# Kernel tuning notes

Measured on AMD Instinct MI355X. Metric: run time of the kernel, lower is better.

The kernel has to match this reference:

```python
import jax, jax.numpy as jnp
import numpy as np

B, S, HID = 2, 2048, 2048
H, KV, D = 16, 8, 128          # query heads, kv heads, head dim
NREP = H // KV
EPS = 1e-6
THETA = 1000000.0
SCALE = 1.0 / np.sqrt(D)


def setup_inputs() -> dict:
    key = jax.random.key(0)
    ks = jax.random.split(key, 5)
    x = jax.random.normal(ks[0], (B, S, HID), jnp.float32)
    std = 0.02
    Wq = jax.random.normal(ks[1], (HID, H * D), jnp.float32) * std
    Wk = jax.random.normal(ks[2], (HID, KV * D), jnp.float32) * std
    Wv = jax.random.normal(ks[3], (HID, KV * D), jnp.float32) * std
    Wo = jax.random.normal(ks[4], (H * D, HID), jnp.float32) * std
    q_norm_w = jnp.ones((D,), jnp.float32)
    k_norm_w = jnp.ones((D,), jnp.float32)
    # standard RoPE cos/sin table: [S, D]
    inv_freq = 1.0 / (THETA ** (jnp.arange(0, D, 2, dtype=jnp.float32) / D))
    freqs = jnp.arange(S, dtype=jnp.float32)[:, None] * inv_freq[None, :]
    emb = jnp.concatenate([freqs, freqs], axis=-1)
    return {"x": x, "Wq": Wq, "Wk": Wk, "Wv": Wv, "Wo": Wo,
            "q_norm_w": q_norm_w, "k_norm_w": k_norm_w,
            "cos": jnp.cos(emb), "sin": jnp.sin(emb)}


def _rmsnorm(x, w, eps=EPS):
    var = jnp.mean(jnp.square(x), axis=-1, keepdims=True)
    return w * (x * jax.lax.rsqrt(var + eps))


def _rotate_half(x):
    x1, x2 = jnp.split(x, 2, axis=-1)
    return jnp.concatenate([-x2, x1], axis=-1)


def _rope(t, cos, sin):
    # t: [B, h, S, D]; cos/sin: [S, D]
    return t * cos[None, None] + _rotate_half(t) * sin[None, None]


def reference(x, Wq, Wk, Wv, Wo, q_norm_w, k_norm_w, cos, sin):
    q = (x @ Wq).reshape(B, S, H, D)
    k = (x @ Wk).reshape(B, S, KV, D)
    v = (x @ Wv).reshape(B, S, KV, D)
    q = _rmsnorm(q, q_norm_w).transpose(0, 2, 1, 3)   # [B, H, S, D]
    k = _rmsnorm(k, k_norm_w).transpose(0, 2, 1, 3)   # [B, KV, S, D]
    v = v.transpose(0, 2, 1, 3)                       # [B, KV, S, D]
    q = _rope(q, cos, sin)
    k = _rope(k, cos, sin)
    # GQA without materializing repeated K/V: group q heads per kv head
    qg = q.reshape(B, KV, NREP, S, D)
    scores = jnp.einsum('bgrsd,bgtd->bgrst', qg, k) * SCALE  # [B,KV,NREP,S,S]
    causal = jnp.tril(jnp.ones((S, S), dtype=bool))
    scores = jnp.where(causal, scores, jnp.finfo(scores.dtype).min)
    p = jax.nn.softmax(scores, axis=-1)
    out = jnp.einsum('bgrst,bgtd->bgrsd', p, v).reshape(B, H, S, D)
    out = out.transpose(0, 2, 1, 3).reshape(B, S, H * D)
    return out @ Wo
```

## Files before the change

kernel.cpp:

```cpp
#include <hip/hip_runtime.h>

typedef unsigned short u16;
typedef __bf16 bf16x8 __attribute__((ext_vector_type(8)));
typedef float f32x4 __attribute__((ext_vector_type(4)));

#define Bn 2
#define Sn 2048
#define HIDn 2048
#define Hn 16
#define KVn 8
#define Dn 128
#define SCALEf 0.08838834764831845f

__device__ __forceinline__ float b2f(u16 v) {
  return __builtin_bit_cast(float, (unsigned)v << 16);
}
__device__ __forceinline__ u16 f2b(float f) {
  unsigned u = __builtin_bit_cast(unsigned, f);
  u += 0x7fffu + ((u >> 16) & 1u);
  return (u16)(u >> 16);
}
__device__ __forceinline__ bool is_bf16(const void* det) {
  return *(const unsigned*)det == 0x3F803F80u;
}
__device__ __forceinline__ float ldx(const void* p, long i, bool isbf) {
  return isbf ? b2f(((const u16*)p)[i]) : ((const float*)p)[i];
}
__device__ __forceinline__ void gl_lds16(const u16* g, u16* l) {
  __builtin_amdgcn_global_load_lds(
      (unsigned int __attribute__((address_space(1)))*)g,
      (unsigned int __attribute__((address_space(3)))*)l, 16, 0, 0);
}

template <int CTRL>
__device__ __forceinline__ float dpp_mov(float x) {
  return __builtin_bit_cast(
      float, __builtin_amdgcn_update_dpp(0, __builtin_bit_cast(int, x), CTRL,
                                         0xF, 0xF, true));
}
__device__ __forceinline__ float red16_max(float x) {
  x = fmaxf(x, dpp_mov<0xB1>(x));
  x = fmaxf(x, dpp_mov<0x4E>(x));
  x = fmaxf(x, dpp_mov<0x141>(x));
  x = fmaxf(x, dpp_mov<0x140>(x));
  return x;
}
__device__ __forceinline__ float red16_sum(float x) {
  x += dpp_mov<0xB1>(x);
  x += dpp_mov<0x4E>(x);
  x += dpp_mov<0x141>(x);
  x += dpp_mov<0x140>(x);
  return x;
}

__global__ __launch_bounds__(256) void convert_x(
    const void* __restrict__ in, u16* __restrict__ out, const void* __restrict__ det) {
  bool isbf = is_bf16(det);
  long i = ((long)blockIdx.x * 256 + threadIdx.x) * 4;
  if (isbf) {
    *(ushort4*)(out + i) = *(const ushort4*)((const u16*)in + i);
  } else {
    float4 f = *(const float4*)((const float*)in + i);
    out[i] = f2b(f.x); out[i + 1] = f2b(f.y); out[i + 2] = f2b(f.z); out[i + 3] = f2b(f.w);
  }
}

__global__ __launch_bounds__(256) void transpose_any(
    const void* __restrict__ vin, u16* __restrict__ out, const void* __restrict__ det,
    int irs, int ors, long ib0, long ob0, int nb1, long ib1, long ob1) {
  __shared__ u16 tile[64][65];
  bool isbf = det ? is_bf16(det) : true;
  int bz = blockIdx.z;
  long ibase = (long)(bz / nb1) * ib0 + (long)(bz % nb1) * ib1;
  u16* op = out + (long)(bz / nb1) * ob0 + (long)(bz % nb1) * ob1;
  long r0 = (long)blockIdx.y * 64, c0 = (long)blockIdx.x * 64;
  int t = threadIdx.x;
  int tr = t >> 3, tc = (t & 7) * 8;
#pragma unroll
  for (int p = 0; p < 2; ++p) {
    int r = p * 32 + tr;
    long src = ibase + (r0 + r) * irs + c0 + tc;
    if (isbf) {
      const u16* ip = (const u16*)vin;
#pragma unroll
      for (int j = 0; j < 8; ++j) tile[r][tc + j] = ip[src + j];
    } else {
      const float* ip = (const float*)vin;
#pragma unroll
      for (int j = 0; j < 8; ++j) tile[r][tc + j] = f2b(ip[src + j]);
    }
  }
  __syncthreads();
#pragma unroll
  for (int p = 0; p < 2; ++p) {
    int r = p * 32 + tr;
    u16* dst = op + (c0 + r) * ors + r0 + tc;
#pragma unroll
    for (int j = 0; j < 8; ++j) dst[j] = tile[tc + j][r];
  }
}

__global__ __launch_bounds__(256) void gemm_bt(
    const u16* __restrict__ A, const u16* __restrict__ Bt, u16* __restrict__ C,
    float* __restrict__ Cf, const void* __restrict__ det, int N, int K) {
  __shared__ alignas(16) u16 As[128 * 64];
  __shared__ alignas(16) u16 Bs[128 * 64];
  int t = threadIdx.x;
  int wave = t >> 6, lane = t & 63, quad = lane >> 4, l15 = lane & 15;
  long bm = (long)blockIdx.y * 128, bn = (long)blockIdx.x * 128;
  int wm = (wave >> 1) * 64, wn = (wave & 1) * 64;
  f32x4 acc[4][4] = {};
  int sg = ((t & 7) ^ ((t >> 3) & 7)) * 8;
  const u16* Ab = A + (bm + (t >> 3)) * K + sg;
  const u16* Bb = Bt + (bn + (t >> 3)) * K + sg;
  for (int k0 = 0; k0 < K; k0 += 64) {
    __syncthreads();
#pragma unroll
    for (int p = 0; p < 4; ++p) {
      gl_lds16(Ab + (long)(p * 32) * K + k0, As + p * 2048 + t * 8);
      gl_lds16(Bb + (long)(p * 32) * K + k0, Bs + p * 2048 + t * 8);
    }
    __syncthreads();
#pragma unroll
    for (int kt = 0; kt < 2; ++kt) {
      int fg = ((kt * 4 + quad) ^ (l15 & 7)) * 8;
      bf16x8 a[4], b[4];
#pragma unroll
      for (int i = 0; i < 4; ++i)
        a[i] = *(const bf16x8*)(As + (wm + i * 16 + l15) * 64 + fg);
#pragma unroll
      for (int j = 0; j < 4; ++j)
        b[j] = *(const bf16x8*)(Bs + (wn + j * 16 + l15) * 64 + fg);
#pragma unroll
      for (int i = 0; i < 4; ++i)
#pragma unroll
        for (int j = 0; j < 4; ++j)
          acc[i][j] = __builtin_amdgcn_mfma_f32_16x16x32_bf16(a[i], b[j], acc[i][j], 0, 0, 0);
    }
  }
  bool tofloat = (Cf != nullptr) && !is_bf16(det);
#pragma unroll
  for (int i = 0; i < 4; ++i) {
    long row = bm + wm + i * 16 + quad * 4;
#pragma unroll
    for (int j = 0; j < 4; ++j) {
      long col = bn + wn + j * 16 + l15;
      if (tofloat) {
#pragma unroll
        for (int r = 0; r < 4; ++r) Cf[(row + r) * N + col] = acc[i][j][r];
      } else {
#pragma unroll
        for (int r = 0; r < 4; ++r) C[(row + r) * N + col] = f2b(acc[i][j][r]);
      }
    }
  }
}

__global__ __launch_bounds__(512, 2) void gemm_qkv256(
    const u16* __restrict__ A, const u16* __restrict__ Bt,
    u16* __restrict__ Qout, u16* __restrict__ Kout, u16* __restrict__ Vout,
    const void* __restrict__ qw, const void* __restrict__ kw,
    const void* __restrict__ cosb, const void* __restrict__ sinb, int K) {
  __shared__ alignas(16) u16 As[2][2][8192];
  __shared__ alignas(16) u16 Bs[2][2][8192];
  const int NT = K >> 6;
  bool isbf = is_bf16(qw);
  int t = threadIdx.x;
  int wave = t >> 6, lane = t & 63, quad = lane >> 4, l15 = lane & 15;
  int l7 = l15 & 7;
  int wmi = wave >> 1, wni = wave & 1;
  long bm = (long)blockIdx.y * 256;
  long bn = (long)blockIdx.x * 256;
  int s0 = t, s1 = t + 512;
  int r0 = s0 >> 3, r1 = s1 >> 3;
  int gs0 = (s0 & 7) ^ (r0 & 7), gs1 = (s1 & 7) ^ (r1 & 7);
  const u16* Ab0 = A + bm * K;
  const u16* Ab1 = A + (bm + 128) * K;
  const u16* Bb0 = Bt + bn * K;
  const u16* Bb1 = Bt + (bn + 128) * K;
#define STG(dst, src)                                          \
  gl_lds16((src) + (long)r0 * K + gs0 * 8, (dst) + s0 * 8);    \
  gl_lds16((src) + (long)r1 * K + gs1 * 8, (dst) + s1 * 8);
#define FENCE asm volatile("" ::: "memory")
  int ah = wmi >> 1;
  int arb = (wmi & 1) * 64 + l15;
#define LDA(m, kk) (*(const bf16x8*)(Ah + (arb + (m)*16) * 64 + ((((kk)*4 + quad) ^ l7) * 8)))
#define LDB(n, kk) (*(const bf16x8*)(Bh + ((n)*16 + l15) * 64 + ((((kk)*4 + quad) ^ l7) * 8)))
  f32x4 acc[4][8] = {};
  STG((u16*)As[0][0], Ab0);
  STG((u16*)As[0][1], Ab1);
  STG((u16*)Bs[0][0], Bb0);
  STG((u16*)Bs[0][1], Bb1);
  STG((u16*)As[1][0], Ab0 + 64);
  STG((u16*)As[1][1], Ab1 + 64);
  asm volatile("s_waitcnt vmcnt(4)" ::: "memory");
  __builtin_amdgcn_s_barrier();

  for (int tk = 0; tk < NT; ++tk) {
    const u16* Ah = (const u16*)As[tk & 1][ah];
    const u16* Bh = (const u16*)Bs[tk & 1][wni];
    u16* BsN0 = (u16*)Bs[(tk + 1) & 1][0];
    u16* BsN1 = (u16*)Bs[(tk + 1) & 1][1];
    u16* AsN0 = (u16*)As[tk & 1][0];
    u16* AsN1 = (u16*)As[tk & 1][1];
    bf16x8 aa[4], bb[4];
#pragma unroll
    for (int m = 0; m < 4; ++m) aa[m] = LDA(m, 0);
#pragma unroll
    for (int j = 0; j < 4; ++j) bb[j] = LDB(j, 0);
    if (tk + 1 < NT) { STG(BsN0, Bb0 + (tk + 1) * 64); }
    FENCE; __builtin_amdgcn_s_barrier();
    asm volatile("s_waitcnt lgkmcnt(0)" ::: "memory");
    __builtin_amdgcn_s_setprio(1);
#pragma unroll
    for (int m = 0; m < 4; ++m)
#pragma unroll
      for (int j = 0; j < 4; ++j)
        acc[m][j] = __builtin_amdgcn_mfma_f32_16x16x32_bf16(aa[m], bb[j], acc[m][j], 0, 0, 0);
    __builtin_amdgcn_s_setprio(0);
    FENCE; __builtin_amdgcn_s_barrier();
#pragma unroll
    for (int j = 0; j < 4; ++j) bb[j] = LDB(j + 4, 0);
    if (tk + 1 < NT) { STG(BsN1, Bb1 + (tk + 1) * 64); }
    FENCE; __builtin_amdgcn_s_barrier();
    asm volatile("s_waitcnt lgkmcnt(0)" ::: "memory");
    __builtin_amdgcn_s_setprio(1);
#pragma unroll
    for (int m = 0; m < 4; ++m)
#pragma unroll
      for (int j = 0; j < 4; ++j)
        acc[m][j + 4] = __builtin_amdgcn_mfma_f32_16x16x32_bf16(aa[m], bb[j], acc[m][j + 4], 0, 0, 0);
    __builtin_amdgcn_s_setprio(0);
    FENCE; __builtin_amdgcn_s_barrier();
#pragma unroll
    for (int m = 0; m < 4; ++m) aa[m] = LDA(m, 1);
#pragma unroll
    for (int j = 0; j < 4; ++j) bb[j] = LDB(j, 1);
    FENCE; __builtin_amdgcn_s_barrier();
    asm volatile("s_waitcnt lgkmcnt(0)" ::: "memory");
    __builtin_amdgcn_s_setprio(1);
#pragma unroll
    for (int m = 0; m < 4; ++m)
#pragma unroll
      for (int j = 0; j < 4; ++j)
        acc[m][j] = __builtin_amdgcn_mfma_f32_16x16x32_bf16(aa[m], bb[j], acc[m][j], 0, 0, 0);
    __builtin_amdgcn_s_setprio(0);
    FENCE; __builtin_amdgcn_s_barrier();
#pragma unroll
    for (int j = 0; j < 4; ++j) bb[j] = LDB(j + 4, 1);
    if (tk + 2 < NT) {
      STG(AsN0, Ab0 + (tk + 2) * 64);
      STG(AsN1, Ab1 + (tk + 2) * 64);
      asm volatile("s_waitcnt vmcnt(4)" ::: "memory");
    } else {
      asm volatile("s_waitcnt vmcnt(0)" ::: "memory");
    }
    __builtin_amdgcn_s_barrier();
    asm volatile("s_waitcnt lgkmcnt(0)" ::: "memory");
    __builtin_amdgcn_s_setprio(1);
#pragma unroll
    for (int m = 0; m < 4; ++m)
#pragma unroll
      for (int j = 0; j < 4; ++j)
        acc[m][j + 4] = __builtin_amdgcn_mfma_f32_16x16x32_bf16(aa[m], bb[j], acc[m][j + 4], 0, 0, 0);
    __builtin_amdgcn_s_setprio(0);
    FENCE; __builtin_amdgcn_s_barrier();
  }
#undef STG
#undef LDA
#undef LDB
#undef FENCE
  int hglob = (int)(bn >> 7) + wni;
  int mrow0 = (int)bm + wmi * 64 + quad * 4;
  if (hglob < Hn + KVn) {
    bool isq = hglob < Hn;
    const void* w = isq ? qw : kw;
    int nh = isq ? Hn : KVn;
    int hh = isq ? hglob : hglob - Hn;
    u16* Ob = isq ? Qout : Kout;
#pragma unroll
    for (int m = 0; m < 4; ++m) {
#pragma unroll
      for (int r = 0; r < 4; ++r) {
        float ss = 0.f;
#pragma unroll
        for (int j = 0; j < 8; ++j) { float v = acc[m][j][r]; ss += v * v; }
        ss = red16_sum(ss);
        float scale = rsqrtf(ss * (1.0f / 128.0f) + 1e-6f);
        int mr = mrow0 + m * 16 + r;
        int b = mr >> 11, s = mr & (Sn - 1);
        u16* dst = Ob + (((long)b * nh + hh) * Sn + s) * Dn;
        long cb = (long)s * Dn;
#pragma unroll
        for (int j = 0; j < 4; ++j) {
          int c1i = j * 16 + l15, c2i = c1i + 64;
          float x1 = acc[m][j][r] * scale * ldx(w, c1i, isbf);
          float x2 = acc[m][j + 4][r] * scale * ldx(w, c2i, isbf);
          float c1 = ldx(cosb, cb + c1i, isbf), s1 = ldx(sinb, cb + c1i, isbf);
          float c2 = ldx(cosb, cb + c2i, isbf), s2 = ldx(sinb, cb + c2i, isbf);
          dst[c1i] = f2b(x1 * c1 - x2 * s1);
          dst[c2i] = f2b(x2 * c2 + x1 * s2);
        }
      }
    }
  } else {
    int kv = hglob - Hn - KVn;
    int bidx = (int)(bm >> 11);
    int srow = ((int)bm & (Sn - 1)) + wmi * 64 + quad * 4;
#pragma unroll
    for (int m = 0; m < 4; ++m) {
      int sb = srow + m * 16;
#pragma unroll
      for (int j = 0; j < 8; ++j) {
        int d = j * 16 + l15;
        ushort4 tmp;
        tmp.x = f2b(acc[m][j][0]);
        tmp.y = f2b(acc[m][j][1]);
        tmp.z = f2b(acc[m][j][2]);
        tmp.w = f2b(acc[m][j][3]);
        *(ushort4*)(Vout + (((long)bidx * KVn + kv) * Dn + d) * Sn + sb) = tmp;
      }
    }
  }
}

__global__ __launch_bounds__(512) void attn_kernel(
    const u16* __restrict__ Qr, const u16* __restrict__ Kr,
    const u16* __restrict__ Vt, u16* __restrict__ Aout) {
  __shared__ alignas(16) u16 Ks[64 * 128];
  __shared__ alignas(16) u16 Vs[128 * 64];
  __shared__ alignas(16) u16 Ps[8][16 * 64];
  int t = threadIdx.x, wave = t >> 6, lane = t & 63, quad = lane >> 4, l15 = lane & 15;
  int bh = blockIdx.y, b = bh >> 4, h = bh & 15, kvh = h >> 1;
  const u16* kbase = Kr + ((long)b * KVn + kvh) * Sn * Dn;
  const u16* vbase = Vt + ((long)b * KVn + kvh) * (long)Dn * Sn;
  int krow = t >> 4;
  int kgr = ((t & 15) ^ (krow & 15)) * 8;
  int vrow = t >> 3;
  int vgr = ((t & 7) ^ (vrow & 7)) * 8;
  u16* ps = (u16*)Ps[wave];

  for (int half = 0; half < 2; ++half) {
    int qt = half == 0 ? (int)blockIdx.x : 15 - (int)blockIdx.x;
    int row0 = qt * 128 + wave * 16;
    const u16* qbase = Qr + (((long)b * Hn + h) * Sn + row0) * Dn;
    bf16x8 aq[4];
#pragma unroll
    for (int kt = 0; kt < 4; ++kt)
      aq[kt] = *(const bf16x8*)(qbase + l15 * Dn + kt * 32 + quad * 8);
    f32x4 o[8] = {};
    float mi[4], li[4];
#pragma unroll
    for (int r = 0; r < 4; ++r) { mi[r] = -1e30f; li[r] = 0.f; }
    int kv_end = qt * 128 + 128;
    for (int kv0 = 0; kv0 < kv_end; kv0 += 64) {
      __syncthreads();
      {
        const u16* kg = kbase + ((long)kv0 + krow) * Dn + kgr;
        gl_lds16(kg, Ks + t * 8);
        gl_lds16(kg + (long)32 * Dn, Ks + 4096 + t * 8);
        const u16* vg = vbase + (long)vrow * Sn + kv0 + vgr;
        gl_lds16(vg, Vs + t * 8);
        gl_lds16(vg + (long)64 * Sn, Vs + 4096 + t * 8);
      }
      __syncthreads();
      if (kv0 <= row0 + 15) {
        f32x4 sc[4] = {};
#pragma unroll
        for (int kt = 0; kt < 4; ++kt) {
          bf16x8 bk[4];
#pragma unroll
          for (int n = 0; n < 4; ++n)
            bk[n] = *(const bf16x8*)(Ks + (n * 16 + l15) * 128 + (((kt * 4 + quad) ^ l15) * 8));
#pragma unroll
          for (int n = 0; n < 4; ++n)
            sc[n] = __builtin_amdgcn_mfma_f32_16x16x32_bf16(aq[kt], bk[n], sc[n], 0, 0, 0);
        }
        f32x4 sv[4];
#pragma unroll
        for (int n = 0; n < 4; ++n)
#pragma unroll
          for (int r = 0; r < 4; ++r) sv[n][r] = sc[n][r] * SCALEf;
        if (kv0 + 63 > row0) {
#pragma unroll
          for (int n = 0; n < 4; ++n) {
            int col = kv0 + n * 16 + l15;
#pragma unroll
            for (int r = 0; r < 4; ++r)
              if (col > row0 + quad * 4 + r) sv[n][r] = -1e30f;
          }
        }
        float alpha[4], pr[4][4];
#pragma unroll
        for (int r = 0; r < 4; ++r) {
          float mx = fmaxf(fmaxf(sv[0][r], sv[1][r]), fmaxf(sv[2][r], sv[3][r]));
          mx = red16_max(mx);
          float mnew = fmaxf(mi[r], mx);
          alpha[r] = __expf(mi[r] - mnew);
          mi[r] = mnew;
          float rs = 0.f;
#pragma unroll
          for (int n = 0; n < 4; ++n) {
            float pv = __expf(sv[n][r] - mnew);
            pr[r][n] = pv;
            rs += pv;
          }
          rs = red16_sum(rs);
          li[r] = li[r] * alpha[r] + rs;
        }
#pragma unroll
        for (int n = 0; n < 8; ++n)
#pragma unroll
          for (int r = 0; r < 4; ++r) o[n][r] *= alpha[r];
#pragma unroll
        for (int n = 0; n < 4; ++n)
#pragma unroll
          for (int r = 0; r < 4; ++r) {
            int prow = quad * 4 + r;
            int pg = (n * 2 + (l15 >> 3)) ^ (prow & 7);
            ps[prow * 64 + pg * 8 + (l15 & 7)] = f2b(pr[r][n]);
          }
#pragma unroll
        for (int kt2 = 0; kt2 < 2; ++kt2) {
          bf16x8 ap = *(const bf16x8*)(ps + l15 * 64 + (((kt2 * 4 + quad) ^ (l15 & 7)) * 8));
#pragma unroll
          for (int n = 0; n < 8; ++n) {
            bf16x8 bv = *(const bf16x8*)(Vs + (n * 16 + l15) * 64 + (((kt2 * 4 + quad) ^ (l15 & 7)) * 8));
            o[n] = __builtin_amdgcn_mfma_f32_16x16x32_bf16(ap, bv, o[n], 0, 0, 0);
          }
        }
      }
    }
#pragma unroll
    for (int r = 0; r < 4; ++r) {
      long s = row0 + quad * 4 + r;
      float inv = 1.0f / li[r];
      u16* dst = Aout + (((long)b * Sn + s) * Hn + h) * Dn;
#pragma unroll
      for (int n = 0; n < 8; ++n) dst[n * 16 + l15] = f2b(o[n][r] * inv);
    }
  }
}

extern "C" void kernel_launch(void* const* d_in, const int* in_sizes, int n_in,
                              void* d_out, int out_size, void* d_ws, size_t ws_size,
                              hipStream_t stream) {
  (void)in_sizes; (void)n_in; (void)out_size; (void)ws_size;
  const void* x    = d_in[0];
  const void* Wq   = d_in[1];
  const void* Wk   = d_in[2];
  const void* Wv   = d_in[3];
  const void* Wo   = d_in[4];
  const void* qw   = d_in[5];
  const void* kw   = d_in[6];
  const void* cosb = d_in[7];
  const void* sinb = d_in[8];
  u16* ws = (u16*)d_ws;
  u16* dsc = (u16*)d_out;

  u16* Qr = dsc + 0;
  u16* Kr = dsc + 8388608;
  u16* Vt = dsc + 12582912;
  u16* xb = ws + 0;
  u16* WT = ws + 8388608;
  dim3 blk(256);
  convert_x<<<dim3(8192), blk, 0, stream>>>(x, xb, qw);
  transpose_any<<<dim3(32, 32, 1), blk, 0, stream>>>(Wq, WT, qw, 2048, 2048, 0, 0, 1, 0, 0);
  transpose_any<<<dim3(16, 32, 1), blk, 0, stream>>>(Wk, WT + (long)2048 * 2048, qw, 1024, 2048, 0, 0, 1, 0, 0);
  transpose_any<<<dim3(16, 32, 1), blk, 0, stream>>>(Wv, WT + (long)3072 * 2048, qw, 1024, 2048, 0, 0, 1, 0, 0);
  gemm_qkv256<<<dim3(16, 16), dim3(512), 0, stream>>>(xb, WT, Qr, Kr, Vt,
                                                      qw, kw, cosb, sinb, 2048);
  u16* attn = ws + 0;
  attn_kernel<<<dim3(8, 32), dim3(512), 0, stream>>>(Qr, Kr, Vt, attn);
  u16* WoT = ws + 8388608;
  transpose_any<<<dim3(32, 32, 1), blk, 0, stream>>>(Wo, WoT, qw, 2048, 2048, 0, 0, 1, 0, 0);
  gemm_bt<<<dim3(16, 32), blk, 0, stream>>>(attn, WoT, (u16*)d_out, (float*)d_out, qw, 2048, 2048);
}
```

Baseline: 360.9 us.

## Simplify QKV GEMM main loop to plain double-buffered prefetch with single barrier

```diff
diff --git a/kernel.cpp b/kernel.cpp
--- a/kernel.cpp
+++ b/kernel.cpp
@@ -181,7 +181,6 @@
 #define STG(dst, src)                                          \
   gl_lds16((src) + (long)r0 * K + gs0 * 8, (dst) + s0 * 8);    \
   gl_lds16((src) + (long)r1 * K + gs1 * 8, (dst) + s1 * 8);
-#define FENCE asm volatile("" ::: "memory")
   int ah = wmi >> 1;
   int arb = (wmi & 1) * 64 + l15;
 #define LDA(m, kk) (*(const bf16x8*)(Ah + (arb + (m)*16) * 64 + ((((kk)*4 + quad) ^ l7) * 8)))
@@ -191,85 +190,46 @@
   STG((u16*)As[0][1], Ab1);
   STG((u16*)Bs[0][0], Bb0);
   STG((u16*)Bs[0][1], Bb1);
-  STG((u16*)As[1][0], Ab0 + 64);
-  STG((u16*)As[1][1], Ab1 + 64);
-  asm volatile("s_waitcnt vmcnt(4)" ::: "memory");
+  asm volatile("s_waitcnt vmcnt(0)" ::: "memory");
   __builtin_amdgcn_s_barrier();
 
   for (int tk = 0; tk < NT; ++tk) {
     const u16* Ah = (const u16*)As[tk & 1][ah];
     const u16* Bh = (const u16*)Bs[tk & 1][wni];
-    u16* BsN0 = (u16*)Bs[(tk + 1) & 1][0];
-    u16* BsN1 = (u16*)Bs[(tk + 1) & 1][1];
-    u16* AsN0 = (u16*)As[tk & 1][0];
-    u16* AsN1 = (u16*)As[tk & 1][1];
-    bf16x8 aa[4], bb[4];
-#pragma unroll
-    for (int m = 0; m < 4; ++m) aa[m] = LDA(m, 0);
-#pragma unroll
-    for (int j = 0; j < 4; ++j) bb[j] = LDB(j, 0);
-    if (tk + 1 < NT) { STG(BsN0, Bb0 + (tk + 1) * 64); }
-    FENCE; __builtin_amdgcn_s_barrier();
-    asm volatile("s_waitcnt lgkmcnt(0)" ::: "memory");
+    int nx = (tk + 1) & 1;
+    if (tk + 1 < NT) {
+      STG((u16*)As[nx][0], Ab0 + (tk + 1) * 64);
+      STG((u16*)As[nx][1], Ab1 + (tk + 1) * 64);
+      STG((u16*)Bs[nx][0], Bb0 + (tk + 1) * 64);
+      STG((u16*)Bs[nx][1], Bb1 + (tk + 1) * 64);
+    }
+    bf16x8 a0[4], a1[4], b0[8], b1[8];
+#pragma unroll
+    for (int m = 0; m < 4; ++m) a0[m] = LDA(m, 0);
+#pragma unroll
+    for (int n = 0; n < 8; ++n) b0[n] = LDB(n, 0);
+#pragma unroll
+    for (int m = 0; m < 4; ++m) a1[m] = LDA(m, 1);
+#pragma unroll
+    for (int n = 0; n < 8; ++n) b1[n] = LDB(n, 1);
     __builtin_amdgcn_s_setprio(1);
 #pragma unroll
     for (int m = 0; m < 4; ++m)
 #pragma unroll
-      for (int j = 0; j < 4; ++j)
-        acc[m][j] = __builtin_amdgcn_mfma_f32_16x16x32_bf16(aa[m], bb[j], acc[m][j], 0, 0, 0);
+      for (int j = 0; j < 8; ++j)
+        acc[m][j] = __builtin_amdgcn_mfma_f32_16x16x32_bf16(a0[m], b0[j], acc[m][j], 0, 0, 0);
+#pragma unroll
+    for (int m = 0; m < 4; ++m)
+#pragma unroll
+      for (int j = 0; j < 8; ++j)
+        acc[m][j] = __builtin_amdgcn_mfma_f32_16x16x32_bf16(a1[m], b1[j], acc[m][j], 0, 0, 0);
     __builtin_amdgcn_s_setprio(0);
-    FENCE; __builtin_amdgcn_s_barrier();
-#pragma unroll
-    for (int j = 0; j < 4; ++j) bb[j] = LDB(j + 4, 0);
-    if (tk + 1 < NT) { STG(BsN1, Bb1 + (tk + 1) * 64); }
-    FENCE; __builtin_amdgcn_s_barrier();
-    asm volatile("s_waitcnt lgkmcnt(0)" ::: "memory");
-    __builtin_amdgcn_s_setprio(1);
-#pragma unroll
-    for (int m = 0; m < 4; ++m)
-#pragma unroll
-      for (int j = 0; j < 4; ++j)
-        acc[m][j + 4] = __builtin_amdgcn_mfma_f32_16x16x32_bf16(aa[m], bb[j], acc[m][j + 4], 0, 0, 0);
-    __builtin_amdgcn_s_setprio(0);
-    FENCE; __builtin_amdgcn_s_barrier();
-#pragma unroll
-    for (int m = 0; m < 4; ++m) aa[m] = LDA(m, 1);
-#pragma unroll
-    for (int j = 0; j < 4; ++j) bb[j] = LDB(j, 1);
-    FENCE; __builtin_amdgcn_s_barrier();
-    asm volatile("s_waitcnt lgkmcnt(0)" ::: "memory");
-    __builtin_amdgcn_s_setprio(1);
-#pragma unroll
-    for (int m = 0; m < 4; ++m)
-#pragma unroll
-      for (int j = 0; j < 4; ++j)
-        acc[m][j] = __builtin_amdgcn_mfma_f32_16x16x32_bf16(aa[m], bb[j], acc[m][j], 0, 0, 0);
-    __builtin_amdgcn_s_setprio(0);
-    FENCE; __builtin_amdgcn_s_barrier();
-#pragma unroll
-    for (int j = 0; j < 4; ++j) bb[j] = LDB(j + 4, 1);
-    if (tk + 2 < NT) {
-      STG(AsN0, Ab0 + (tk + 2) * 64);
-      STG(AsN1, Ab1 + (tk + 2) * 64);
-      asm volatile("s_waitcnt vmcnt(4)" ::: "memory");
-    } else {
-      asm volatile("s_waitcnt vmcnt(0)" ::: "memory");
-    }
+    asm volatile("s_waitcnt vmcnt(0)" ::: "memory");
     __builtin_amdgcn_s_barrier();
-    asm volatile("s_waitcnt lgkmcnt(0)" ::: "memory");
-    __builtin_amdgcn_s_setprio(1);
-#pragma unroll
-    for (int m = 0; m < 4; ++m)
-#pragma unroll
-      for (int j = 0; j < 4; ++j)
-        acc[m][j + 4] = __builtin_amdgcn_mfma_f32_16x16x32_bf16(aa[m], bb[j], acc[m][j + 4], 0, 0, 0);
-    __builtin_amdgcn_s_setprio(0);
-    FENCE; __builtin_amdgcn_s_barrier();
   }
 #undef STG
 #undef LDA
 #undef LDB
-#undef FENCE
   int hglob = (int)(bn >> 7) + wni;
   int mrow0 = (int)bm + wmi * 64 + quad * 4;
   if (hglob < Hn + KVn) {
```

Result: no change. 366.4 us (+1.5%).
